# Kernel optimization log

Hardware: AMD Instinct MI355X
Metric: run time of the kernel (lower is better)

The kernel has to match this reference:

```python
import jax, jax.numpy as jnp
import numpy as np

D, H, C, T, B = 1024, 128, 256, 16, 8192


def setup_inputs() -> dict:
    key = jax.random.key(0)
    ks = jax.random.split(key, 7)
    s = 0.02
    return {
        "x": jax.random.normal(ks[0], (B, D), dtype=jnp.float32),
        "Wr": jax.random.normal(ks[1], (D, T), dtype=jnp.float32) * s,  # router weight (transposed vs torch)
        "br": jnp.zeros((T,), dtype=jnp.float32),
        "W1": jax.random.normal(ks[2], (T, D, H), dtype=jnp.float32) * s,  # per-task fc1
        "b1": jnp.zeros((T, H), dtype=jnp.float32),
        "W2": jax.random.normal(ks[3], (T, H, C), dtype=jnp.float32) * s,  # per-task fc2
        "b2": jnp.zeros((T, C), dtype=jnp.float32),
    }


def reference(x, Wr, br, W1, b1, W2, b2):
    # Router: softmax over tasks, [B, T]
    task_probs = jax.nn.softmax(x @ Wr + br, axis=1)
    # All task experts as one batched grouped-GEMM pass.
    h = jax.nn.relu(jnp.einsum("bd,tdh->tbh", x, W1) + b1[:, None, :])  # [T, B, H]
    preds = jnp.einsum("tbh,thc->tbc", h, W2) + b2[:, None, :]           # [T, B, C]
    # Weight each task's predictions by its routing probability.
    task_preds = preds * task_probs.T[:, :, None]                         # [T, B, C]
    return task_probs, task_preds
```

## Files before the change

kernel.cpp:

```cpp
#include <hip/hip_runtime.h>

using bf16x8 = __attribute__((ext_vector_type(8))) short;
using f32x4  = __attribute__((ext_vector_type(4))) float;

#define B_SZ 8192
#define D_SZ 1024
#define H_SZ 128
#define C_SZ 256
#define T_SZ 16

__device__ __forceinline__ unsigned short f2bf(float f) {
  unsigned int u = __float_as_uint(f);
  return (unsigned short)((u + 0x7fffu + ((u >> 16) & 1u)) >> 16);
}

__global__ __launch_bounds__(256) void transpose_cast_kernel(const float* __restrict__ src,
                                                             unsigned short* __restrict__ dst,
                                                             int R, int C, int cshift) {
  __shared__ float tile[32][257];
  const int t = blockIdx.y;
  const int r0 = blockIdx.x * 32;
  const float* s = src + ((size_t)t * R + r0) * C;
  const int n = 32 * C;
  for (int idx = threadIdx.x; idx < n; idx += 256)
    tile[idx >> cshift][idx & (C - 1)] = s[idx];
  __syncthreads();
  unsigned short* d = dst + (size_t)t * C * R + r0;
  for (int idx = threadIdx.x; idx < n; idx += 256) {
    int cc = idx >> 5, rr = idx & 31;
    d[(size_t)cc * R + rr] = f2bf(tile[rr][cc]);
  }
}

__global__ __launch_bounds__(256) void router_cast_kernel(const float* __restrict__ x,
                                                          const float* __restrict__ Wr,
                                                          const float* __restrict__ br,
                                                          float* __restrict__ out0,
                                                          unsigned short* __restrict__ xb) {
  const int lane = threadIdx.x & 63;
  const int wid  = threadIdx.x >> 6;
  const int brow = blockIdx.x * 16 + wid * 4;
  float acc[4][16];
#pragma unroll
  for (int r = 0; r < 4; ++r)
#pragma unroll
    for (int tt = 0; tt < 16; ++tt) acc[r][tt] = 0.f;

  for (int it = 0; it < 16; ++it) {
    const int d = it * 64 + lane;
    const float4* w4 = (const float4*)(Wr + (size_t)d * 16);
    float4 wa = w4[0], wb = w4[1], wc = w4[2], wd = w4[3];
    const float wv[16] = {wa.x, wa.y, wa.z, wa.w, wb.x, wb.y, wb.z, wb.w,
                          wc.x, wc.y, wc.z, wc.w, wd.x, wd.y, wd.z, wd.w};
#pragma unroll
    for (int r = 0; r < 4; ++r) {
      const float xv = x[(size_t)(brow + r) * 1024 + d];
      xb[(size_t)(brow + r) * 1024 + d] = f2bf(xv);
#pragma unroll
      for (int tt = 0; tt < 16; ++tt) acc[r][tt] += xv * wv[tt];
    }
  }
#pragma unroll
  for (int off = 32; off >= 1; off >>= 1) {
#pragma unroll
    for (int r = 0; r < 4; ++r)
#pragma unroll
      for (int tt = 0; tt < 16; ++tt) acc[r][tt] += __shfl_xor(acc[r][tt], off);
  }
  if (lane == 0) {
#pragma unroll
    for (int r = 0; r < 4; ++r) {
      float v[16]; float m = -1e30f;
#pragma unroll
      for (int tt = 0; tt < 16; ++tt) { v[tt] = acc[r][tt] + br[tt]; m = fmaxf(m, v[tt]); }
      float ssum = 0.f;
#pragma unroll
      for (int tt = 0; tt < 16; ++tt) { v[tt] = __expf(v[tt] - m); ssum += v[tt]; }
      const float inv = 1.0f / ssum;
      float4* o = (float4*)(out0 + (size_t)(brow + r) * 16);
      o[0] = make_float4(v[0] * inv, v[1] * inv, v[2] * inv, v[3] * inv);
      o[1] = make_float4(v[4] * inv, v[5] * inv, v[6] * inv, v[7] * inv);
      o[2] = make_float4(v[8] * inv, v[9] * inv, v[10] * inv, v[11] * inv);
      o[3] = make_float4(v[12] * inv, v[13] * inv, v[14] * inv, v[15] * inv);
    }
  }
}

__global__ __launch_bounds__(256, 2) void expert_kernel(
    const unsigned short* __restrict__ xb, const unsigned short* __restrict__ w1b,
    const unsigned short* __restrict__ w2b, const float* __restrict__ b1,
    const float* __restrict__ b2, const float* __restrict__ probs,
    float* __restrict__ out1) {
  __shared__ __align__(16) char smem[65536];
  const int tid  = threadIdx.x;
  const int lane = tid & 63;
  const int w    = tid >> 6;
  const int l16  = lane & 15;
  const int l4   = lane >> 4;

  const int bid  = blockIdx.x;
  const int xcd  = bid & 7;
  const int i    = bid >> 3;
  const int ngrp = i & 7;
  const int mloc = i >> 3;
  const int t0   = ngrp * 2;
  const int b0   = (xcd * 8 + mloc) * 128;

  const int wm = w >> 1;
  const int wn = w & 1;
  const int t  = t0 + wn;

  unsigned int goff[8], ldo[8];
#pragma unroll
  for (int it = 0; it < 8; ++it) {
    const unsigned int o = (unsigned int)it * 4096u + (unsigned int)tid * 16u;
    const unsigned int row = o >> 7;
    const unsigned int cb  = (o & 127u) ^ ((row & 7u) << 4);
    goff[it] = row * 1024u + (cb >> 1);
    ldo[it]  = o;
  }
  const unsigned short* w1base = w1b + (size_t)t0 * 128 * 1024;

#define STAGE(curbuf, kt)                                                              \
  {                                                                                    \
    _Pragma("unroll")                                                                  \
    for (int it = 0; it < 8; ++it) {                                                   \
      const unsigned short* g = w1base + goff[it] + (kt) * 64;                         \
      char* dd = smem + (curbuf) * 32768 + (int)ldo[it];                               \
      __builtin_amdgcn_global_load_lds(                                                \
          (const __attribute__((address_space(1))) unsigned int*)g,                    \
          (__attribute__((address_space(3))) unsigned int*)dd, 16, 0, 0);              \
    }                                                                                  \
  }

  const unsigned short* xr = xb + (size_t)(b0 + wm * 64 + l16) * 1024 + l4 * 8;

  f32x4 acc1[8][4] = {};

  STAGE(0, 0);
  __syncthreads();
  int buf = 0;
  for (int kt = 0; kt < 16; ++kt) {
    if (kt < 15) STAGE(buf ^ 1, kt + 1);
    bf16x8 bx[2][4];
#pragma unroll
    for (int ks = 0; ks < 2; ++ks)
#pragma unroll
      for (int mi = 0; mi < 4; ++mi)
        bx[ks][mi] = *(const bf16x8*)(xr + mi * 16384 + kt * 64 + ks * 32);
#pragma unroll
    for (int ks = 0; ks < 2; ++ks) {
      bf16x8 aw[8];
#pragma unroll
      for (int ni = 0; ni < 8; ++ni) {
        const int row = wn * 128 + ni * 16 + l16;
        aw[ni] = *(const bf16x8*)(smem + buf * 32768 + (row << 7) +
                                  ((ks * 64 + l4 * 16) ^ ((row & 7) << 4)));
      }
      __builtin_amdgcn_s_setprio(1);
#pragma unroll
      for (int ni = 0; ni < 8; ++ni)
#pragma unroll
        for (int mi = 0; mi < 4; ++mi)
          acc1[ni][mi] = __builtin_amdgcn_mfma_f32_16x16x32_bf16(aw[ni], bx[ks][mi], acc1[ni][mi], 0, 0, 0);
      __builtin_amdgcn_s_setprio(0);
    }
    __syncthreads();
    buf ^= 1;
  }

#pragma unroll
  for (int ni = 0; ni < 8; ++ni) {
    const int n0 = ni * 16 + l4 * 4;
    float bb[4];
#pragma unroll
    for (int r = 0; r < 4; ++r) bb[r] = b1[t * 128 + n0 + r];
#pragma unroll
    for (int mi = 0; mi < 4; ++mi) {
      const int m = wm * 64 + mi * 16 + l16;
      unsigned int pk[2];
#pragma unroll
      for (int h = 0; h < 2; ++h) {
        float v0 = fmaxf(acc1[ni][mi][2 * h + 0] + bb[2 * h + 0], 0.f);
        float v1 = fmaxf(acc1[ni][mi][2 * h + 1] + bb[2 * h + 1], 0.f);
        pk[h] = (unsigned int)f2bf(v0) | ((unsigned int)f2bf(v1) << 16);
      }
      const int inner = (wn * 256 + n0 * 2) ^ ((m & 7) << 4);
      *(uint2*)(smem + (m << 9) + inner) = make_uint2(pk[0], pk[1]);
    }
  }
  __syncthreads();

  const unsigned short* w2t = w2b + (size_t)t * C_SZ * H_SZ;
  const size_t outbase = (size_t)t * (size_t)(B_SZ * C_SZ);
#pragma unroll
  for (int ch = 0; ch < 2; ++ch) {
    f32x4 acc2[4][8] = {};
#pragma unroll
    for (int ks = 0; ks < 4; ++ks) {
      bf16x8 ah[4];
#pragma unroll
      for (int mi = 0; mi < 4; ++mi) {
        const int row = wm * 64 + mi * 16 + l16;
        const int inner = (wn * 256 + ks * 64 + l4 * 16) ^ ((row & 7) << 4);
        ah[mi] = *(const bf16x8*)(smem + (row << 9) + inner);
      }
#pragma unroll
      for (int ci = 0; ci < 8; ++ci) {
        const int c = ch * 128 + ci * 16 + l16;
        bf16x8 bw = *(const bf16x8*)(w2t + (size_t)c * 128 + ks * 32 + l4 * 8);
#pragma unroll
        for (int mi = 0; mi < 4; ++mi)
          acc2[mi][ci] = __builtin_amdgcn_mfma_f32_16x16x32_bf16(ah[mi], bw, acc2[mi][ci], 0, 0, 0);
      }
    }
#pragma unroll
    for (int mi = 0; mi < 4; ++mi) {
      const int m0 = wm * 64 + mi * 16 + l4 * 4;
      float pv[4];
#pragma unroll
      for (int r = 0; r < 4; ++r) pv[r] = probs[(size_t)(b0 + m0 + r) * 16 + t];
#pragma unroll
      for (int ci = 0; ci < 8; ++ci) {
        const int c = ch * 128 + ci * 16 + l16;
        const float bias = b2[t * 256 + c];
#pragma unroll
        for (int r = 0; r < 4; ++r)
          out1[outbase + (size_t)(b0 + m0 + r) * 256 + c] = (acc2[mi][ci][r] + bias) * pv[r];
      }
    }
  }
}

extern "C" void kernel_launch(void* const* d_in, const int* in_sizes, int n_in,
                              void* d_out, int out_size, void* d_ws, size_t ws_size,
                              hipStream_t stream) {
  const float* x  = (const float*)d_in[0];
  const float* Wr = (const float*)d_in[1];
  const float* br = (const float*)d_in[2];
  const float* W1 = (const float*)d_in[3];
  const float* b1 = (const float*)d_in[4];
  const float* W2 = (const float*)d_in[5];
  const float* b2 = (const float*)d_in[6];
  float* out0 = (float*)d_out;
  float* out1 = out0 + (size_t)B_SZ * T_SZ;

  char* ws = (char*)d_ws;
  unsigned short* xb  = (unsigned short*)ws;
  unsigned short* w1b = (unsigned short*)(ws + (size_t)16777216);
  unsigned short* w2b = (unsigned short*)(ws + (size_t)16777216 + 4194304);

  router_cast_kernel<<<B_SZ / 16, 256, 0, stream>>>(x, Wr, br, out0, xb);
  transpose_cast_kernel<<<dim3(D_SZ / 32, T_SZ), 256, 0, stream>>>(W1, w1b, D_SZ, H_SZ, 7);
  transpose_cast_kernel<<<dim3(H_SZ / 32, T_SZ), 256, 0, stream>>>(W2, w2b, H_SZ, C_SZ, 8);
  expert_kernel<<<512, 256, 0, stream>>>(xb, w1b, w2b, b1, b2, out0, out1);
}
```

Baseline: 115.8 us.

## Enlarge expert block to 256 rows and stage x tiles through LDS

The expert kernel now uses 512-thread blocks that each cover 256 batch rows and two tasks. Both the x tile and the W1 tile are staged into double-buffered LDS with async global-to-LDS loads, so all waves share them instead of each wave reading x straight from global memory. The h fragments and routing probabilities for the second GEMM are also hoisted out of its loops. In exchange, LDS use grows to 128KB per block, which limits residency to one block per CU, and the launch bound of 512 threads with 2 blocks may squeeze the register budget enough to spill the large accumulator arrays.

```diff
diff --git a/kernel.cpp b/kernel.cpp
--- a/kernel.cpp
+++ b/kernel.cpp
@@ -86,12 +86,14 @@
   }
 }
 
-__global__ __launch_bounds__(256, 2) void expert_kernel(
+#define SW_OFF 65536
+
+__global__ __launch_bounds__(512, 2) void expert_kernel(
     const unsigned short* __restrict__ xb, const unsigned short* __restrict__ w1b,
     const unsigned short* __restrict__ w2b, const float* __restrict__ b1,
     const float* __restrict__ b2, const float* __restrict__ probs,
     float* __restrict__ out1) {
-  __shared__ __align__(16) char smem[65536];
+  __shared__ __align__(16) char smem[131072];
   const int tid  = threadIdx.x;
   const int lane = tid & 63;
   const int w    = tid >> 6;
@@ -100,74 +102,81 @@
 
   const int bid  = blockIdx.x;
   const int xcd  = bid & 7;
-  const int i    = bid >> 3;
-  const int ngrp = i & 7;
-  const int mloc = i >> 3;
-  const int t0   = ngrp * 2;
-  const int b0   = (xcd * 8 + mloc) * 128;
-
-  const int wm = w >> 1;
-  const int wn = w & 1;
-  const int t  = t0 + wn;
-
-  unsigned int goff[8], ldo[8];
+  const int j    = bid >> 3;
+  const int tp   = j & 7;
+  const int mloc = j >> 3;
+  const int t0   = tp * 2;
+  const int b0   = (xcd * 4 + mloc) * 256;
+
+  const unsigned short* gp[8];
+  unsigned int ldo[8];
 #pragma unroll
   for (int it = 0; it < 8; ++it) {
-    const unsigned int o = (unsigned int)it * 4096u + (unsigned int)tid * 16u;
+    const unsigned int o = (unsigned int)(it & 3) * 8192u + (unsigned int)tid * 16u;
     const unsigned int row = o >> 7;
     const unsigned int cb  = (o & 127u) ^ ((row & 7u) << 4);
-    goff[it] = row * 1024u + (cb >> 1);
-    ldo[it]  = o;
-  }
-  const unsigned short* w1base = w1b + (size_t)t0 * 128 * 1024;
+    if (it < 4) gp[it] = xb + (size_t)(b0 + row) * 1024 + (cb >> 1);
+    else        gp[it] = w1b + ((size_t)(t0 + (row >> 7)) * 128 + (row & 127u)) * 1024 + (cb >> 1);
+    ldo[it] = o;
+  }
 
 #define STAGE(curbuf, kt)                                                              \
   {                                                                                    \
     _Pragma("unroll")                                                                  \
     for (int it = 0; it < 8; ++it) {                                                   \
-      const unsigned short* g = w1base + goff[it] + (kt) * 64;                         \
-      char* dd = smem + (curbuf) * 32768 + (int)ldo[it];                               \
+      const unsigned short* g = gp[it] + (kt) * 64;                                    \
+      char* dd = smem + (it < 4 ? (curbuf) * 32768 + (int)ldo[it]                      \
+                                : SW_OFF + (curbuf) * 32768 + (int)ldo[it]);           \
       __builtin_amdgcn_global_load_lds(                                                \
           (const __attribute__((address_space(1))) unsigned int*)g,                    \
           (__attribute__((address_space(3))) unsigned int*)dd, 16, 0, 0);              \
     }                                                                                  \
   }
 
-  const unsigned short* xr = xb + (size_t)(b0 + wm * 64 + l16) * 1024 + l4 * 8;
-
+  const int wn = w & 1;
+  const int wm = w >> 1;
+  const int t  = t0 + wn;
   f32x4 acc1[8][4] = {};
 
+#define FC1_COMPUTE(curbuf)                                                            \
+  {                                                                                    \
+    const int bx_base = (curbuf) * 32768;                                              \
+    const int aw_base = SW_OFF + (curbuf) * 32768;                                     \
+    _Pragma("unroll")                                                                  \
+    for (int ks = 0; ks < 2; ++ks) {                                                   \
+      const int cb = ks * 64 + l4 * 16;                                                \
+      bf16x8 aw[8], bx[4];                                                             \
+      _Pragma("unroll")                                                                \
+      for (int ni = 0; ni < 8; ++ni) {                                                 \
+        const int row = wn * 128 + ni * 16 + l16;                                      \
+        aw[ni] = *(const bf16x8*)(smem + aw_base + (row << 7) + (cb ^ ((row & 7) << 4)));\
+      }                                                                                \
+      _Pragma("unroll")                                                                \
+      for (int mi = 0; mi < 4; ++mi) {                                                 \
+        const int row = wm * 64 + mi * 16 + l16;                                       \
+        bx[mi] = *(const bf16x8*)(smem + bx_base + (row << 7) + (cb ^ ((row & 7) << 4)));\
+      }                                                                                \
+      __builtin_amdgcn_s_setprio(1);                                                   \
+      _Pragma("unroll")                                                                \
+      for (int ni = 0; ni < 8; ++ni)                                                   \
+        _Pragma("unroll")                                                              \
+        for (int mi = 0; mi < 4; ++mi)                                                 \
+          acc1[ni][mi] = __builtin_amdgcn_mfma_f32_16x16x32_bf16(aw[ni], bx[mi], acc1[ni][mi], 0, 0, 0); \
+      __builtin_amdgcn_s_setprio(0);                                                   \
+    }                                                                                  \
+  }
+
   STAGE(0, 0);
   __syncthreads();
-  int buf = 0;
-  for (int kt = 0; kt < 16; ++kt) {
-    if (kt < 15) STAGE(buf ^ 1, kt + 1);
-    bf16x8 bx[2][4];
-#pragma unroll
-    for (int ks = 0; ks < 2; ++ks)
-#pragma unroll
-      for (int mi = 0; mi < 4; ++mi)
-        bx[ks][mi] = *(const bf16x8*)(xr + mi * 16384 + kt * 64 + ks * 32);
-#pragma unroll
-    for (int ks = 0; ks < 2; ++ks) {
-      bf16x8 aw[8];
-#pragma unroll
-      for (int ni = 0; ni < 8; ++ni) {
-        const int row = wn * 128 + ni * 16 + l16;
-        aw[ni] = *(const bf16x8*)(smem + buf * 32768 + (row << 7) +
-                                  ((ks * 64 + l4 * 16) ^ ((row & 7) << 4)));
-      }
-      __builtin_amdgcn_s_setprio(1);
-#pragma unroll
-      for (int ni = 0; ni < 8; ++ni)
-#pragma unroll
-        for (int mi = 0; mi < 4; ++mi)
-          acc1[ni][mi] = __builtin_amdgcn_mfma_f32_16x16x32_bf16(aw[ni], bx[ks][mi], acc1[ni][mi], 0, 0, 0);
-      __builtin_amdgcn_s_setprio(0);
-    }
+  int cur = 0;
+  for (int kt = 0; kt < 15; ++kt) {
+    STAGE(cur ^ 1, kt + 1);
+    FC1_COMPUTE(cur);
     __syncthreads();
-    buf ^= 1;
-  }
+    cur ^= 1;
+  }
+  FC1_COMPUTE(cur);
+  __syncthreads();
 
 #pragma unroll
   for (int ni = 0; ni < 8; ++ni) {
@@ -193,40 +202,49 @@
 
   const unsigned short* w2t = w2b + (size_t)t * C_SZ * H_SZ;
   const size_t outbase = (size_t)t * (size_t)(B_SZ * C_SZ);
+
+  bf16x8 ah[4][4];
+#pragma unroll
+  for (int ks = 0; ks < 4; ++ks)
+#pragma unroll
+    for (int mi = 0; mi < 4; ++mi) {
+      const int row = wm * 64 + mi * 16 + l16;
+      const int inner = (wn * 256 + ks * 64 + l4 * 16) ^ ((row & 7) << 4);
+      ah[ks][mi] = *(const bf16x8*)(smem + (row << 9) + inner);
+    }
+
+  float pv[4][4];
+#pragma unroll
+  for (int mi = 0; mi < 4; ++mi) {
+    const int m0 = wm * 64 + mi * 16 + l4 * 4;
+#pragma unroll
+    for (int r = 0; r < 4; ++r) pv[mi][r] = probs[(size_t)(b0 + m0 + r) * 16 + t];
+  }
+
 #pragma unroll
   for (int ch = 0; ch < 2; ++ch) {
     f32x4 acc2[4][8] = {};
 #pragma unroll
     for (int ks = 0; ks < 4; ++ks) {
-      bf16x8 ah[4];
-#pragma unroll
-      for (int mi = 0; mi < 4; ++mi) {
-        const int row = wm * 64 + mi * 16 + l16;
-        const int inner = (wn * 256 + ks * 64 + l4 * 16) ^ ((row & 7) << 4);
-        ah[mi] = *(const bf16x8*)(smem + (row << 9) + inner);
-      }
 #pragma unroll
       for (int ci = 0; ci < 8; ++ci) {
         const int c = ch * 128 + ci * 16 + l16;
         bf16x8 bw = *(const bf16x8*)(w2t + (size_t)c * 128 + ks * 32 + l4 * 8);
 #pragma unroll
         for (int mi = 0; mi < 4; ++mi)
-          acc2[mi][ci] = __builtin_amdgcn_mfma_f32_16x16x32_bf16(ah[mi], bw, acc2[mi][ci], 0, 0, 0);
+          acc2[mi][ci] = __builtin_amdgcn_mfma_f32_16x16x32_bf16(ah[ks][mi], bw, acc2[mi][ci], 0, 0, 0);
       }
     }
 #pragma unroll
     for (int mi = 0; mi < 4; ++mi) {
       const int m0 = wm * 64 + mi * 16 + l4 * 4;
-      float pv[4];
-#pragma unroll
-      for (int r = 0; r < 4; ++r) pv[r] = probs[(size_t)(b0 + m0 + r) * 16 + t];
 #pragma unroll
       for (int ci = 0; ci < 8; ++ci) {
         const int c = ch * 128 + ci * 16 + l16;
         const float bias = b2[t * 256 + c];
 #pragma unroll
         for (int r = 0; r < 4; ++r)
-          out1[outbase + (size_t)(b0 + m0 + r) * 256 + c] = (acc2[mi][ci][r] + bias) * pv[r];
+          out1[outbase + (size_t)(b0 + m0 + r) * 256 + c] = (acc2[mi][ci][r] + bias) * pv[mi][r];
       }
     }
   }
@@ -253,5 +271,5 @@
   router_cast_kernel<<<B_SZ / 16, 256, 0, stream>>>(x, Wr, br, out0, xb);
   transpose_cast_kernel<<<dim3(D_SZ / 32, T_SZ), 256, 0, stream>>>(W1, w1b, D_SZ, H_SZ, 7);
   transpose_cast_kernel<<<dim3(H_SZ / 32, T_SZ), 256, 0, stream>>>(W2, w2b, H_SZ, C_SZ, 8);
-  expert_kernel<<<512, 256, 0, stream>>>(xb, w1b, w2b, b1, b2, out0, out1);
-}
+  expert_kernel<<<256, 512, 0, stream>>>(xb, w1b, w2b, b1, b2, out0, out1);
+}
```

After: 112.4 us. -3.0%, faster.
